# Performance work log

Measured on AMD Instinct MI355X. Metric: run time of the kernel, lower is better.

Reference implementation:

```python
import jax, jax.numpy as jnp
import numpy as np

C_IN, C_OUT, K, DG, PAD = 256, 256, 3, 2, 1
EPS = 1e-5


def setup_inputs() -> dict:
    key = jax.random.key(0)
    k = jax.random.split(key, 8)
    B, H, W = 4, 64, 64
    x = jax.random.normal(k[0], (B, C_IN, H, W), jnp.float32)
    # offset/mask conv (DCNv2 pack): 3 * dg * k * k output channels
    w_off = jax.random.normal(k[1], (3 * DG * K * K, C_IN, K, K), jnp.float32) * 0.01
    b_off = jnp.zeros((3 * DG * K * K,), jnp.float32)
    # main deformable conv weight
    w = jax.random.normal(k[2], (C_OUT, C_IN, K, K), jnp.float32) * (1.0 / np.sqrt(C_IN * K * K))
    b = jnp.zeros((C_OUT,), jnp.float32)
    # BatchNorm (eval mode: running stats)
    gamma = jnp.ones((C_OUT,), jnp.float32)
    beta = jnp.zeros((C_OUT,), jnp.float32)
    running_mean = jax.random.normal(k[3], (C_OUT,), jnp.float32) * 0.1
    running_var = jax.random.uniform(k[4], (C_OUT,), jnp.float32, 0.5, 1.5)
    return dict(x=x, w_off=w_off, b_off=b_off, w=w, b=b, gamma=gamma, beta=beta,
                running_mean=running_mean, running_var=running_var)


def _conv2d_same(x, w, b):
    y = jax.lax.conv_general_dilated(x, w, (1, 1), 'SAME',
                                     dimension_numbers=('NCHW', 'OIHW', 'NCHW'))
    return y + b[None, :, None, None]


def _deform_conv(x, w_off, b_off, w, b):
    B, C, H, W = x.shape
    K2 = K * K
    Cg = C // DG
    # offsets + modulation mask from internal conv (DCNv2 pack)
    om = _conv2d_same(x, w_off, b_off)            # [B, 3*DG*K2, H, W]
    o1, o2, m = jnp.split(om, 3, axis=1)
    mask = jax.nn.sigmoid(m).reshape(B, DG, 1, K2, H * W)
    off_y = o1.reshape(B, DG, K2, H, W)
    off_x = o2.reshape(B, DG, K2, H, W)
    # base sampling grid: output pixel + kernel tap - pad
    ki = jnp.arange(K)
    ky = (jnp.repeat(ki, K) - PAD).astype(jnp.float32)   # [K2]
    kx = (jnp.tile(ki, K) - PAD).astype(jnp.float32)     # [K2]
    py = off_y + ky[:, None, None] + jnp.arange(H, dtype=jnp.float32)[None, :, None]
    px = off_x + kx[:, None, None] + jnp.arange(W, dtype=jnp.float32)[None, None, :]
    y0 = jnp.floor(py)
    x0 = jnp.floor(px)
    ly = (py - y0).reshape(B, DG, 1, K2, H * W)
    lx = (px - x0).reshape(B, DG, 1, K2, H * W)
    y0i = y0.astype(jnp.int32)
    x0i = x0.astype(jnp.int32)
    xg = x.reshape(B, DG, Cg, H * W)

    def gather(yi, xi):
        # zero-padded bilinear corner gather, per deformable group
        valid = (yi >= 0) & (yi < H) & (xi >= 0) & (xi < W)
        lin = jnp.clip(yi, 0, H - 1) * W + jnp.clip(xi, 0, W - 1)
        v = jnp.take_along_axis(xg[:, :, :, None, :],
                                lin.reshape(B, DG, 1, K2, H * W), axis=-1)
        return v * valid.reshape(B, DG, 1, K2, H * W)

    val = (gather(y0i, x0i) * (1 - ly) * (1 - lx)
           + gather(y0i, x0i + 1) * (1 - ly) * lx
           + gather(y0i + 1, x0i) * ly * (1 - lx)
           + gather(y0i + 1, x0i + 1) * ly * lx)
    val = val * mask                               # [B, DG, Cg, K2, H*W]
    wr = w.reshape(C_OUT, DG, Cg, K2)
    out = jnp.einsum('bgckn,ogck->bon', val, wr).reshape(B, C_OUT, H, W)
    return out + b[None, :, None, None]


def reference(x, w_off, b_off, w, b, gamma, beta, running_mean, running_var):
    y = _deform_conv(x, w_off, b_off, w, b)
    inv = gamma / jnp.sqrt(running_var + EPS)
    y = (y - running_mean[None, :, None, None]) * inv[None, :, None, None] + beta[None, :, None, None]
    return jax.nn.relu(y)
```

## Files before the change

kernel.cpp:

```cpp
#include <hip/hip_runtime.h>
#include <math.h>

typedef __bf16 bf16x8 __attribute__((ext_vector_type(8)));
typedef float  f32x4  __attribute__((ext_vector_type(4)));
typedef int    i32x4  __attribute__((ext_vector_type(4)));

#define MFMA16(a, b, c) __builtin_amdgcn_mfma_f32_16x16x32_bf16((a), (b), (c), 0, 0, 0)

#define ATIDX(r, c) ((r) * 128 + (((c) ^ ((r) & 7)) * 8))

__global__ __launch_bounds__(256) void xpose_kernel(
    const float* __restrict__ x, __bf16* __restrict__ xT) {
  __shared__ float xs[64][65];
  int t = threadIdx.x;
  int b = blockIdx.x >> 8, y = (blockIdx.x >> 2) & 63, cc = blockIdx.x & 3;
  for (int i = t; i < 4096; i += 256) {
    int cl = i >> 6, xc = i & 63;
    xs[cl][xc] = x[(((size_t)b * 256 + cc * 64 + cl) * 64 + y) * 64 + xc];
  }
  __syncthreads();
  for (int i = t; i < 4096; i += 256) {
    int xc = i >> 6, cl = i & 63;
    xT[(((size_t)b * 64 + y) * 64 + xc) * 256 + cc * 64 + cl] = (__bf16)xs[cl][xc];
  }
}

__global__ __launch_bounds__(256) void prep_kernel(
    const float* __restrict__ w, const float* __restrict__ w_off,
    const float* __restrict__ bconv, const float* __restrict__ gamma,
    const float* __restrict__ beta, const float* __restrict__ mean,
    const float* __restrict__ var,
    __bf16* __restrict__ wFragD, __bf16* __restrict__ wFragO,
    float* __restrict__ sc, float* __restrict__ sh) {
  int i = blockIdx.x * 256 + threadIdx.x;
  if (i < 589824) {
    int j = i & 7, lane = (i >> 3) & 63, ocb = (i >> 9) & 15;
    int kc = (i >> 13) & 3, gk = i >> 15;
    int klocal = (lane >> 4) * 8 + j;
    int oc = ocb * 16 + (lane & 15);
    int c = kc * 32 + klocal;
    int g = gk / 9, ktap = gk % 9;
    wFragD[i] = (__bf16)w[((size_t)oc * 256 + g * 128 + c) * 9 + ktap];
  } else {
    int i2 = i - 589824;
    int j = i2 & 7, lane = (i2 >> 3) & 63, ocb = (i2 >> 9) & 3;
    int kc = (i2 >> 11) & 7, tap = i2 >> 14;
    int klocal = (lane >> 4) * 8 + j;
    int oc = ocb * 16 + (lane & 15);
    int ci = kc * 32 + klocal;
    wFragO[i2] = (oc < 54) ? (__bf16)w_off[((size_t)oc * 256 + ci) * 9 + tap]
                           : (__bf16)0.f;
  }
  if (i < 256) {
    float s = gamma[i] * rsqrtf(var[i] + 1e-5f);
    sc[i] = s;
    sh[i] = (bconv[i] - mean[i]) * s + beta[i];
  }
}

__global__ __launch_bounds__(512) void offconv_kernel(
    const __bf16* __restrict__ xT, const __bf16* __restrict__ wFragO,
    const float* __restrict__ b_off, float* __restrict__ om) {
  __shared__ __attribute__((aligned(16))) __bf16 rowbuf[3 * 66 * 256];
  int t = threadIdx.x;
  int b = blockIdx.x >> 6, y = blockIdx.x & 63;
  int lane = t & 63, wv = t >> 6;
  int l15 = lane & 15, quad = lane >> 4;
  int mh = wv & 1, ocq = wv >> 1;
  const __bf16* xTb = xT + (size_t)b * 64 * 64 * 256;
  bf16x8 z8;
  #pragma unroll
  for (int e = 0; e < 8; ++e) z8[e] = (__bf16)0.f;

  for (int i = t; i < 3 * 66 * 32; i += 512) {
    int c = i & 31, px66 = (i >> 5) % 66, dy = i / 2112;
    int y2 = y + dy - 1, x2 = px66 - 1;
    bf16x8 v = z8;
    if (y2 >= 0 && y2 < 64 && x2 >= 0 && x2 < 64)
      v = *(const bf16x8*)(xTb + ((size_t)y2 * 64 + x2) * 256 + c * 8);
    *(bf16x8*)&rowbuf[dy * 16896 + px66 * 256 + ((c ^ (px66 & 7)) * 8)] = v;
  }
  __syncthreads();

  f32x4 acc0 = {0.f, 0.f, 0.f, 0.f};
  f32x4 acc1 = {0.f, 0.f, 0.f, 0.f};
  for (int tap = 0; tap < 9; ++tap) {
    int dy = tap / 3, dxs = tap % 3;
    const __bf16* bb = wFragO + ((size_t)(tap * 8) * 4 + ocq) * 512 + lane * 8;
    bf16x8 Bf[8];
    #pragma unroll
    for (int kc = 0; kc < 8; ++kc)
      Bf[kc] = *(const bf16x8*)(bb + (size_t)kc * 4 * 512);
    int p0 = mh * 32 + l15 + dxs, p1 = p0 + 16;
    const __bf16* rb = rowbuf + dy * 16896;
    #pragma unroll
    for (int kc = 0; kc < 8; ++kc) {
      int c = kc * 4 + quad;
      bf16x8 a0 = *(const bf16x8*)&rb[p0 * 256 + ((c ^ (p0 & 7)) * 8)];
      bf16x8 a1 = *(const bf16x8*)&rb[p1 * 256 + ((c ^ (p1 & 7)) * 8)];
      acc0 = MFMA16(a0, Bf[kc], acc0);
      acc1 = MFMA16(a1, Bf[kc], acc1);
    }
  }

  int oc = ocq * 16 + l15;
  if (oc < 54) {
    float bo = b_off[oc];
    #pragma unroll
    for (int fm = 0; fm < 2; ++fm) {
      f32x4 v = fm ? acc1 : acc0;
      f32x4 r = {v.x + bo, v.y + bo, v.z + bo, v.w + bo};
      int pxs = mh * 32 + fm * 16 + quad * 4;
      *(f32x4*)(om + (((size_t)b * 54 + oc) * 64 + y) * 64 + pxs) = r;
    }
  }
}

__global__ __launch_bounds__(512) void dconv_kernel(
    const __bf16* __restrict__ xT, const float* __restrict__ om,
    const __bf16* __restrict__ wFragD, const float* __restrict__ sc,
    const float* __restrict__ sh, float* __restrict__ out) {
  __shared__ f32x4 swgtv[18 * 64];
  __shared__ i32x4 slinv[18 * 64];
  __shared__ __attribute__((aligned(16))) __bf16 atile[2][64 * 128];
  int t = threadIdx.x;
  int b = blockIdx.x >> 6, y = blockIdx.x & 63;
  int lane = t & 63, wv = t >> 6;
  int l15 = lane & 15, quad = lane >> 4;
  const __bf16* xTb = xT + (size_t)b * 64 * 64 * 256;

  for (int i = t; i < 18 * 64; i += 512) {
    int gk = i >> 6, p = i & 63;
    int k = gk % 9;
    size_t obase = (size_t)b * 54 * 4096 + (size_t)y * 64 + p;
    float oy = om[obase + (size_t)gk * 4096];
    float ox = om[obase + (size_t)(18 + gk) * 4096];
    float mz = om[obase + (size_t)(36 + gk) * 4096];
    float mv = 1.f / (1.f + expf(-mz));
    float py  = (float)(y + (k / 3) - 1) + oy;
    float pxf = (float)(p + (k % 3) - 1) + ox;
    float y0f = floorf(py), x0f = floorf(pxf);
    int y0 = (int)y0f, x0 = (int)x0f;
    float ly = py - y0f, lx = pxf - x0f;
    int y1 = y0 + 1, x1 = x0 + 1;
    bool vy0 = (y0 >= 0) && (y0 < 64), vy1 = (y1 >= 0) && (y1 < 64);
    bool vx0 = (x0 >= 0) && (x0 < 64), vx1 = (x1 >= 0) && (x1 < 64);
    int cy0 = min(max(y0, 0), 63), cy1 = min(max(y1, 0), 63);
    int cx0 = min(max(x0, 0), 63), cx1 = min(max(x1, 0), 63);
    f32x4 sv;
    sv.x = (vy0 && vx0) ? (1.f - ly) * (1.f - lx) * mv : 0.f;
    sv.y = (vy0 && vx1) ? (1.f - ly) * lx * mv : 0.f;
    sv.z = (vy1 && vx0) ? ly * (1.f - lx) * mv : 0.f;
    sv.w = (vy1 && vx1) ? ly * lx * mv : 0.f;
    i32x4 lv;
    lv.x = (cy0 * 64 + cx0) * 256;
    lv.y = (cy0 * 64 + cx1) * 256;
    lv.z = (cy1 * 64 + cx0) * 256;
    lv.w = (cy1 * 64 + cx1) * 256;
    swgtv[i] = sv;
    slinv[i] = lv;
  }

  f32x4 acc[4][2];
  #pragma unroll
  for (int fm = 0; fm < 4; ++fm)
    #pragma unroll
    for (int fn = 0; fn < 2; ++fn)
      acc[fm][fn] = (f32x4){0.f, 0.f, 0.f, 0.f};

  __syncthreads();

  int ch0 = l15 * 8;
  {
    const __bf16* xg = xTb + ch0;
    #pragma unroll
    for (int j = 0; j < 2; ++j) {
      int p = wv * 8 + j * 4 + quad;
      f32x4 sv = swgtv[p];
      i32x4 lv = slinv[p];
      bf16x8 c0 = *(const bf16x8*)(xg + lv.x);
      bf16x8 c1 = *(const bf16x8*)(xg + lv.y);
      bf16x8 c2 = *(const bf16x8*)(xg + lv.z);
      bf16x8 c3 = *(const bf16x8*)(xg + lv.w);
      bf16x8 o;
      #pragma unroll
      for (int e = 0; e < 8; ++e)
        o[e] = (__bf16)(sv.x * (float)c0[e] + sv.y * (float)c1[e]
                      + sv.z * (float)c2[e] + sv.w * (float)c3[e]);
      *(bf16x8*)&atile[0][ATIDX(p, l15)] = o;
    }
  }
  bf16x8 Bf[8];
  {
    const __bf16* bb = wFragD + ((size_t)wv * 2) * 512 + lane * 8;
    #pragma unroll
    for (int kc = 0; kc < 4; ++kc) {
      Bf[kc * 2]     = *(const bf16x8*)(bb + (size_t)kc * 16 * 512);
      Bf[kc * 2 + 1] = *(const bf16x8*)(bb + (size_t)kc * 16 * 512 + 512);
    }
  }

  for (int gk = 0; gk < 18; ++gk) {
    __syncthreads();
    bf16x8 cr[2][4];
    f32x4 sv[2];
    int pj[2];
    if (gk < 17) {
      int gn = gk + 1;
      const __bf16* xg = xTb + (gn / 9) * 128 + ch0;
      #pragma unroll
      for (int j = 0; j < 2; ++j) {
        int p = wv * 8 + j * 4 + quad;
        pj[j] = p;
        sv[j] = swgtv[gn * 64 + p];
        i32x4 lv = slinv[gn * 64 + p];
        cr[j][0] = *(const bf16x8*)(xg + lv.x);
        cr[j][1] = *(const bf16x8*)(xg + lv.y);
        cr[j][2] = *(const bf16x8*)(xg + lv.z);
        cr[j][3] = *(const bf16x8*)(xg + lv.w);
      }
    }
    const __bf16* at = atile[gk & 1];
    #pragma unroll
    for (int kc = 0; kc < 4; ++kc) {
      #pragma unroll
      for (int fm = 0; fm < 4; ++fm) {
        bf16x8 a = *(const bf16x8*)&at[ATIDX(fm * 16 + l15, kc * 4 + quad)];
        acc[fm][0] = MFMA16(a, Bf[kc * 2],     acc[fm][0]);
        acc[fm][1] = MFMA16(a, Bf[kc * 2 + 1], acc[fm][1]);
      }
    }
    if (gk < 17) {
      __bf16* dst = atile[(gk + 1) & 1];
      #pragma unroll
      for (int j = 0; j < 2; ++j) {
        bf16x8 o;
        #pragma unroll
        for (int e = 0; e < 8; ++e)
          o[e] = (__bf16)(sv[j].x * (float)cr[j][0][e] + sv[j].y * (float)cr[j][1][e]
                        + sv[j].z * (float)cr[j][2][e] + sv[j].w * (float)cr[j][3][e]);
        *(bf16x8*)&dst[ATIDX(pj[j], l15)] = o;
      }
      const __bf16* bb = wFragD + ((size_t)((gk + 1) * 4) * 16 + wv * 2) * 512 + lane * 8;
      #pragma unroll
      for (int kc = 0; kc < 4; ++kc) {
        Bf[kc * 2]     = *(const bf16x8*)(bb + (size_t)kc * 16 * 512);
        Bf[kc * 2 + 1] = *(const bf16x8*)(bb + (size_t)kc * 16 * 512 + 512);
      }
    }
  }

  #pragma unroll
  for (int fm = 0; fm < 4; ++fm) {
    #pragma unroll
    for (int fn = 0; fn < 2; ++fn) {
      int oc = wv * 32 + fn * 16 + l15;
      float s = sc[oc], h = sh[oc];
      f32x4 v = acc[fm][fn];
      f32x4 r = {fmaxf(v.x * s + h, 0.f), fmaxf(v.y * s + h, 0.f),
                 fmaxf(v.z * s + h, 0.f), fmaxf(v.w * s + h, 0.f)};
      int pxs = fm * 16 + quad * 4;
      *(f32x4*)(out + (((size_t)b * 256 + oc) * 64 + y) * 64 + pxs) = r;
    }
  }
}

extern "C" void kernel_launch(void* const* d_in, const int* in_sizes, int n_in,
                              void* d_out, int out_size, void* d_ws, size_t ws_size,
                              hipStream_t stream) {
  const float* x     = (const float*)d_in[0];
  const float* w_off = (const float*)d_in[1];
  const float* b_off = (const float*)d_in[2];
  const float* w     = (const float*)d_in[3];
  const float* bconv = (const float*)d_in[4];
  const float* gamma = (const float*)d_in[5];
  const float* beta  = (const float*)d_in[6];
  const float* rmean = (const float*)d_in[7];
  const float* rvar  = (const float*)d_in[8];
  float* out = (float*)d_out;

  float*  om     = (float*)d_ws;
  __bf16* xT     = (__bf16*)((char*)d_ws + 3538944);
  __bf16* wFragD = (__bf16*)((char*)d_ws + 11927552);
  __bf16* wFragO = (__bf16*)((char*)d_ws + 13107200);
  float*  sc     = (float*)((char*)d_ws + 13402112);
  float*  sh     = (float*)((char*)d_ws + 13403136);

  xpose_kernel<<<4 * 64 * 4, 256, 0, stream>>>(x, xT);
  prep_kernel<<<2880, 256, 0, stream>>>(w, w_off, bconv, gamma, beta, rmean, rvar,
                                        wFragD, wFragO, sc, sh);
  offconv_kernel<<<4 * 64, 512, 0, stream>>>(xT, wFragO, b_off, om);
  dconv_kernel<<<4 * 64, 512, 0, stream>>>(xT, om, wFragD, sc, sh, out);
}
```

Before: 138.2 us.

## Fuse offset conv into deformable conv kernel and merge setup kernels

Merges the transpose and weight-prep kernels into one launch, and fuses the offset/mask convolution into the deformable-conv kernel. Each block now keeps its row of offsets in LDS instead of writing them to global memory and reading them back. The LDS for the two phases is shared through a union, and an extra 54x64 float buffer holds the offsets. This removes two launches and the global round-trip for the offsets. The cost is one more barrier and higher LDS use per block, which may reduce occupancy.

```diff
diff --git a/kernel.cpp b/kernel.cpp
--- a/kernel.cpp
+++ b/kernel.cpp
@@ -9,30 +9,30 @@
 
 #define ATIDX(r, c) ((r) * 128 + (((c) ^ ((r) & 7)) * 8))
 
-__global__ __launch_bounds__(256) void xpose_kernel(
-    const float* __restrict__ x, __bf16* __restrict__ xT) {
-  __shared__ float xs[64][65];
+__global__ __launch_bounds__(256) void setup_kernel(
+    const float* __restrict__ x, const float* __restrict__ w,
+    const float* __restrict__ w_off, const float* __restrict__ bconv,
+    const float* __restrict__ gamma, const float* __restrict__ beta,
+    const float* __restrict__ mean, const float* __restrict__ var,
+    __bf16* __restrict__ xT, __bf16* __restrict__ wFragD,
+    __bf16* __restrict__ wFragO, float* __restrict__ sc,
+    float* __restrict__ sh) {
   int t = threadIdx.x;
-  int b = blockIdx.x >> 8, y = (blockIdx.x >> 2) & 63, cc = blockIdx.x & 3;
-  for (int i = t; i < 4096; i += 256) {
-    int cl = i >> 6, xc = i & 63;
-    xs[cl][xc] = x[(((size_t)b * 256 + cc * 64 + cl) * 64 + y) * 64 + xc];
-  }
-  __syncthreads();
-  for (int i = t; i < 4096; i += 256) {
-    int xc = i >> 6, cl = i & 63;
-    xT[(((size_t)b * 64 + y) * 64 + xc) * 256 + cc * 64 + cl] = (__bf16)xs[cl][xc];
-  }
-}
-
-__global__ __launch_bounds__(256) void prep_kernel(
-    const float* __restrict__ w, const float* __restrict__ w_off,
-    const float* __restrict__ bconv, const float* __restrict__ gamma,
-    const float* __restrict__ beta, const float* __restrict__ mean,
-    const float* __restrict__ var,
-    __bf16* __restrict__ wFragD, __bf16* __restrict__ wFragO,
-    float* __restrict__ sc, float* __restrict__ sh) {
-  int i = blockIdx.x * 256 + threadIdx.x;
+  if (blockIdx.x < 1024) {
+    __shared__ float xs[64][65];
+    int b = blockIdx.x >> 8, y = (blockIdx.x >> 2) & 63, cc = blockIdx.x & 3;
+    for (int i = t; i < 4096; i += 256) {
+      int cl = i >> 6, xc = i & 63;
+      xs[cl][xc] = x[(((size_t)b * 256 + cc * 64 + cl) * 64 + y) * 64 + xc];
+    }
+    __syncthreads();
+    for (int i = t; i < 4096; i += 256) {
+      int xc = i >> 6, cl = i & 63;
+      xT[(((size_t)b * 64 + y) * 64 + xc) * 256 + cc * 64 + cl] = (__bf16)xs[cl][xc];
+    }
+    return;
+  }
+  int i = (blockIdx.x - 1024) * 256 + t;
   if (i < 589824) {
     int j = i & 7, lane = (i >> 3) & 63, ocb = (i >> 9) & 15;
     int kc = (i >> 13) & 3, gk = i >> 15;
@@ -58,15 +58,27 @@
   }
 }
 
-__global__ __launch_bounds__(512) void offconv_kernel(
-    const __bf16* __restrict__ xT, const __bf16* __restrict__ wFragO,
-    const float* __restrict__ b_off, float* __restrict__ om) {
-  __shared__ __attribute__((aligned(16))) __bf16 rowbuf[3 * 66 * 256];
+struct PhaseC {
+  f32x4 swgtv[18 * 64];
+  i32x4 slinv[18 * 64];
+  __bf16 atile[2][64 * 128];
+};
+union FusedLDS {
+  __bf16 rowbuf[3 * 66 * 256];
+  PhaseC c;
+};
+
+__global__ __launch_bounds__(512) void fused_kernel(
+    const __bf16* __restrict__ xT, const __bf16* __restrict__ wFragD,
+    const __bf16* __restrict__ wFragO, const float* __restrict__ b_off,
+    const float* __restrict__ sc, const float* __restrict__ sh,
+    float* __restrict__ out) {
+  __shared__ __attribute__((aligned(16))) FusedLDS U;
+  __shared__ float omrow[54 * 64];
   int t = threadIdx.x;
   int b = blockIdx.x >> 6, y = blockIdx.x & 63;
   int lane = t & 63, wv = t >> 6;
   int l15 = lane & 15, quad = lane >> 4;
-  int mh = wv & 1, ocq = wv >> 1;
   const __bf16* xTb = xT + (size_t)b * 64 * 64 * 256;
   bf16x8 z8;
   #pragma unroll
@@ -78,64 +90,52 @@
     bf16x8 v = z8;
     if (y2 >= 0 && y2 < 64 && x2 >= 0 && x2 < 64)
       v = *(const bf16x8*)(xTb + ((size_t)y2 * 64 + x2) * 256 + c * 8);
-    *(bf16x8*)&rowbuf[dy * 16896 + px66 * 256 + ((c ^ (px66 & 7)) * 8)] = v;
+    *(bf16x8*)&U.rowbuf[dy * 16896 + px66 * 256 + ((c ^ (px66 & 7)) * 8)] = v;
   }
   __syncthreads();
 
-  f32x4 acc0 = {0.f, 0.f, 0.f, 0.f};
-  f32x4 acc1 = {0.f, 0.f, 0.f, 0.f};
-  for (int tap = 0; tap < 9; ++tap) {
-    int dy = tap / 3, dxs = tap % 3;
-    const __bf16* bb = wFragO + ((size_t)(tap * 8) * 4 + ocq) * 512 + lane * 8;
-    bf16x8 Bf[8];
-    #pragma unroll
-    for (int kc = 0; kc < 8; ++kc)
-      Bf[kc] = *(const bf16x8*)(bb + (size_t)kc * 4 * 512);
-    int p0 = mh * 32 + l15 + dxs, p1 = p0 + 16;
-    const __bf16* rb = rowbuf + dy * 16896;
-    #pragma unroll
-    for (int kc = 0; kc < 8; ++kc) {
-      int c = kc * 4 + quad;
-      bf16x8 a0 = *(const bf16x8*)&rb[p0 * 256 + ((c ^ (p0 & 7)) * 8)];
-      bf16x8 a1 = *(const bf16x8*)&rb[p1 * 256 + ((c ^ (p1 & 7)) * 8)];
-      acc0 = MFMA16(a0, Bf[kc], acc0);
-      acc1 = MFMA16(a1, Bf[kc], acc1);
-    }
-  }
-
-  int oc = ocq * 16 + l15;
-  if (oc < 54) {
-    float bo = b_off[oc];
-    #pragma unroll
-    for (int fm = 0; fm < 2; ++fm) {
-      f32x4 v = fm ? acc1 : acc0;
-      f32x4 r = {v.x + bo, v.y + bo, v.z + bo, v.w + bo};
-      int pxs = mh * 32 + fm * 16 + quad * 4;
-      *(f32x4*)(om + (((size_t)b * 54 + oc) * 64 + y) * 64 + pxs) = r;
-    }
-  }
-}
-
-__global__ __launch_bounds__(512) void dconv_kernel(
-    const __bf16* __restrict__ xT, const float* __restrict__ om,
-    const __bf16* __restrict__ wFragD, const float* __restrict__ sc,
-    const float* __restrict__ sh, float* __restrict__ out) {
-  __shared__ f32x4 swgtv[18 * 64];
-  __shared__ i32x4 slinv[18 * 64];
-  __shared__ __attribute__((aligned(16))) __bf16 atile[2][64 * 128];
-  int t = threadIdx.x;
-  int b = blockIdx.x >> 6, y = blockIdx.x & 63;
-  int lane = t & 63, wv = t >> 6;
-  int l15 = lane & 15, quad = lane >> 4;
-  const __bf16* xTb = xT + (size_t)b * 64 * 64 * 256;
+  {
+    int mh = wv & 1, ocq = wv >> 1;
+    f32x4 acc0 = {0.f, 0.f, 0.f, 0.f};
+    f32x4 acc1 = {0.f, 0.f, 0.f, 0.f};
+    for (int tap = 0; tap < 9; ++tap) {
+      int dy = tap / 3, dxs = tap % 3;
+      const __bf16* bb = wFragO + ((size_t)(tap * 8) * 4 + ocq) * 512 + lane * 8;
+      bf16x8 Bf[8];
+      #pragma unroll
+      for (int kc = 0; kc < 8; ++kc)
+        Bf[kc] = *(const bf16x8*)(bb + (size_t)kc * 4 * 512);
+      int p0 = mh * 32 + l15 + dxs, p1 = p0 + 16;
+      const __bf16* rb = U.rowbuf + dy * 16896;
+      #pragma unroll
+      for (int kc = 0; kc < 8; ++kc) {
+        int c = kc * 4 + quad;
+        bf16x8 a0 = *(const bf16x8*)&rb[p0 * 256 + ((c ^ (p0 & 7)) * 8)];
+        bf16x8 a1 = *(const bf16x8*)&rb[p1 * 256 + ((c ^ (p1 & 7)) * 8)];
+        acc0 = MFMA16(a0, Bf[kc], acc0);
+        acc1 = MFMA16(a1, Bf[kc], acc1);
+      }
+    }
+    int oc = ocq * 16 + l15;
+    if (oc < 54) {
+      float bo = b_off[oc];
+      #pragma unroll
+      for (int fm = 0; fm < 2; ++fm) {
+        f32x4 v = fm ? acc1 : acc0;
+        f32x4 r = {v.x + bo, v.y + bo, v.z + bo, v.w + bo};
+        int pxs = mh * 32 + fm * 16 + quad * 4;
+        *(f32x4*)&omrow[oc * 64 + pxs] = r;
+      }
+    }
+  }
+  __syncthreads();
 
   for (int i = t; i < 18 * 64; i += 512) {
     int gk = i >> 6, p = i & 63;
     int k = gk % 9;
-    size_t obase = (size_t)b * 54 * 4096 + (size_t)y * 64 + p;
-    float oy = om[obase + (size_t)gk * 4096];
-    float ox = om[obase + (size_t)(18 + gk) * 4096];
-    float mz = om[obase + (size_t)(36 + gk) * 4096];
+    float oy = omrow[gk * 64 + p];
+    float ox = omrow[(18 + gk) * 64 + p];
+    float mz = omrow[(36 + gk) * 64 + p];
     float mv = 1.f / (1.f + expf(-mz));
     float py  = (float)(y + (k / 3) - 1) + oy;
     float pxf = (float)(p + (k % 3) - 1) + ox;
@@ -157,8 +157,8 @@
     lv.y = (cy0 * 64 + cx1) * 256;
     lv.z = (cy1 * 64 + cx0) * 256;
     lv.w = (cy1 * 64 + cx1) * 256;
-    swgtv[i] = sv;
-    slinv[i] = lv;
+    U.c.swgtv[i] = sv;
+    U.c.slinv[i] = lv;
   }
 
   f32x4 acc[4][2];
@@ -176,8 +176,8 @@
     #pragma unroll
     for (int j = 0; j < 2; ++j) {
       int p = wv * 8 + j * 4 + quad;
-      f32x4 sv = swgtv[p];
-      i32x4 lv = slinv[p];
+      f32x4 sv = U.c.swgtv[p];
+      i32x4 lv = U.c.slinv[p];
       bf16x8 c0 = *(const bf16x8*)(xg + lv.x);
       bf16x8 c1 = *(const bf16x8*)(xg + lv.y);
       bf16x8 c2 = *(const bf16x8*)(xg + lv.z);
@@ -187,7 +187,7 @@
       for (int e = 0; e < 8; ++e)
         o[e] = (__bf16)(sv.x * (float)c0[e] + sv.y * (float)c1[e]
                       + sv.z * (float)c2[e] + sv.w * (float)c3[e]);
-      *(bf16x8*)&atile[0][ATIDX(p, l15)] = o;
+      *(bf16x8*)&U.c.atile[0][ATIDX(p, l15)] = o;
     }
   }
   bf16x8 Bf[8];
@@ -212,15 +212,15 @@
       for (int j = 0; j < 2; ++j) {
         int p = wv * 8 + j * 4 + quad;
         pj[j] = p;
-        sv[j] = swgtv[gn * 64 + p];
-        i32x4 lv = slinv[gn * 64 + p];
+        sv[j] = U.c.swgtv[gn * 64 + p];
+        i32x4 lv = U.c.slinv[gn * 64 + p];
         cr[j][0] = *(const bf16x8*)(xg + lv.x);
         cr[j][1] = *(const bf16x8*)(xg + lv.y);
         cr[j][2] = *(const bf16x8*)(xg + lv.z);
         cr[j][3] = *(const bf16x8*)(xg + lv.w);
       }
     }
-    const __bf16* at = atile[gk & 1];
+    const __bf16* at = U.c.atile[gk & 1];
     #pragma unroll
     for (int kc = 0; kc < 4; ++kc) {
       #pragma unroll
@@ -231,7 +231,7 @@
       }
     }
     if (gk < 17) {
-      __bf16* dst = atile[(gk + 1) & 1];
+      __bf16* dst = U.c.atile[(gk + 1) & 1];
       #pragma unroll
       for (int j = 0; j < 2; ++j) {
         bf16x8 o;
@@ -279,16 +279,13 @@
   const float* rvar  = (const float*)d_in[8];
   float* out = (float*)d_out;
 
-  float*  om     = (float*)d_ws;
-  __bf16* xT     = (__bf16*)((char*)d_ws + 3538944);
-  __bf16* wFragD = (__bf16*)((char*)d_ws + 11927552);
-  __bf16* wFragO = (__bf16*)((char*)d_ws + 13107200);
-  float*  sc     = (float*)((char*)d_ws + 13402112);
-  float*  sh     = (float*)((char*)d_ws + 13403136);
-
-  xpose_kernel<<<4 * 64 * 4, 256, 0, stream>>>(x, xT);
-  prep_kernel<<<2880, 256, 0, stream>>>(w, w_off, bconv, gamma, beta, rmean, rvar,
-                                        wFragD, wFragO, sc, sh);
-  offconv_kernel<<<4 * 64, 512, 0, stream>>>(xT, wFragO, b_off, om);
-  dconv_kernel<<<4 * 64, 512, 0, stream>>>(xT, om, wFragD, sc, sh, out);
+  __bf16* xT     = (__bf16*)d_ws;
+  __bf16* wFragD = (__bf16*)((char*)d_ws + 8388608);
+  __bf16* wFragO = (__bf16*)((char*)d_ws + 9568256);
+  float*  sc     = (float*)((char*)d_ws + 9863168);
+  float*  sh     = (float*)((char*)d_ws + 9864192);
+
+  setup_kernel<<<1024 + 2880, 256, 0, stream>>>(
+      x, w, w_off, bconv, gamma, beta, rmean, rvar, xT, wFragD, wFragO, sc, sh);
+  fused_kernel<<<4 * 64, 512, 0, stream>>>(xT, wFragD, wFragO, b_off, sc, sh, out);
 }
```

Measured after the change: 131.5 us. 1.05x faster.
